# Performance work log

Hardware: AMD Instinct MI355X
Metric: run time of the kernel (lower is better)

Reference implementation:

```python
import jax, jax.numpy as jnp
import numpy as np

B, N, IN_NF, EDGE_NF = 2, 512, 3, 1
DIM, HEADS, DHEAD, DEPTH = 256, 8, 32, 2
INNER = HEADS * DHEAD
SCALE = DHEAD ** -0.5


def _layernorm(x, g, b):
    m = jnp.mean(x, axis=-1, keepdims=True)
    v = jnp.mean((x - m) ** 2, axis=-1, keepdims=True)
    return (x - m) / jnp.sqrt(v + 1e-5) * g + b


def _rotate_half(x):
    x1, x2 = jnp.split(x, 2, axis=-1)
    return jnp.concatenate([-x2, x1], axis=-1)


def _rotary_freqs(n):
    inv_freq = 1.0 / (10000.0 ** (jnp.arange(0, DHEAD, 2, dtype=jnp.float32) / DHEAD))
    f = jnp.einsum('i,j->ij', jnp.arange(n, dtype=jnp.float32), inv_freq)
    return jnp.concatenate([f, f], axis=-1)  # [n, DHEAD]


def _apply_rotary(freqs, t):
    return t * jnp.cos(freqs) + _rotate_half(t) * jnp.sin(freqs)


def _cdist(x):
    # pairwise L2 distances with grad-safe sqrt at zero (matches torch.cdist fwd)
    d2 = jnp.sum((x[:, :, None, :] - x[:, None, :, :]) ** 2, axis=-1)
    safe = jnp.where(d2 > 0.0, d2, 1.0)
    return jnp.where(d2 > 0.0, jnp.sqrt(safe), 0.0)


def setup_inputs():
    key = jax.random.key(0)
    ks = jax.random.split(key, 12)
    w = lambda k, *shape: jax.random.normal(k, shape, dtype=jnp.float32) * 0.02
    return dict(
        x=jax.random.normal(ks[0], (B, N, IN_NF), dtype=jnp.float32),
        t=jax.random.uniform(ks[1], (B, N, 1), dtype=jnp.float32),
        W_enc=w(ks[2], IN_NF + 1, DIM),
        W_dec=w(ks[3], DIM, IN_NF),
        ln_g=jnp.ones((DEPTH, DIM), jnp.float32),
        ln_b=jnp.zeros((DEPTH, DIM), jnp.float32),
        Wq=w(ks[4], DEPTH, DIM, INNER),
        bq=jnp.zeros((DEPTH, INNER), jnp.float32),
        Wkv=w(ks[5], DEPTH, DIM, 2 * INNER),
        bkv=jnp.zeros((DEPTH, 2 * INNER), jnp.float32),
        We=w(ks[6], DEPTH, EDGE_NF, INNER),
        be=jnp.zeros((DEPTH, INNER), jnp.float32),
        Wo=w(ks[7], DEPTH, INNER, DIM),
        bo=jnp.zeros((DEPTH, DIM), jnp.float32),
        Wg=w(ks[8], DEPTH, 3 * DIM, 1),
    )


def _forward(x, t, W_enc, W_dec, ln_g, ln_b, Wq, bq, Wkv, bkv, We, be, Wo, bo, Wg):
    b, n, _ = x.shape
    edges = _cdist(x)[..., None]                         # [B,N,N,1]
    nodes = jnp.concatenate([x, t], axis=-1) @ W_enc     # [B,N,DIM]
    freqs = _rotary_freqs(n)
    for l in range(DEPTH):
        h = _layernorm(nodes, ln_g[l], ln_b[l])          # PreNorm
        q = (h @ Wq[l] + bq[l]).reshape(b, n, HEADS, DHEAD).transpose(0, 2, 1, 3)
        k, v = jnp.split(h @ Wkv[l] + bkv[l], 2, axis=-1)
        k = k.reshape(b, n, HEADS, DHEAD).transpose(0, 2, 1, 3)
        v = v.reshape(b, n, HEADS, DHEAD).transpose(0, 2, 1, 3)
        e = (edges @ We[l] + be[l]).reshape(b, n, n, HEADS, DHEAD)  # [B,i,j,H,D]
        q = _apply_rotary(freqs, q)
        k = _apply_rotary(freqs, k)
        # sim = q . (k_j + e_ij); split to avoid an extra [B,H,N,N,D] materialization
        sim = (jnp.einsum('bhid,bhjd->bhij', q, k)
               + jnp.einsum('bhid,bijhd->bhij', q, e)) * SCALE
        attn = jax.nn.softmax(sim, axis=-1)
        # out = attn . (v_j + e_ij)
        out = (jnp.einsum('bhij,bhjd->bhid', attn, v)
               + jnp.einsum('bhij,bijhd->bhid', attn, e))
        out = out.transpose(0, 2, 1, 3).reshape(b, n, INNER) @ Wo[l] + bo[l]
        # gated residual
        gate = jax.nn.sigmoid(
            jnp.concatenate([out, nodes, out - nodes], axis=-1) @ Wg[l])
        nodes = out * gate + nodes * (1.0 - gate)
    return nodes @ W_dec                                  # [B,N,IN_NF]


def reference(x, t, W_enc, W_dec, ln_g, ln_b, Wq, bq, Wkv, bkv, We, be, Wo, bo, Wg):
    return _forward(x, t, W_enc, W_dec, ln_g, ln_b, Wq, bq, Wkv, bkv, We, be, Wo, bo, Wg)
```

## Files before the change

kernel.cpp:

```cpp
#include <hip/hip_runtime.h>
#include <math.h>

#define B 2
#define N 512
#define DIM 256
#define HEADS 8
#define DHEAD 32
#define INNER 256
#define DEPTH 2
#define SCALE 0.17677669529663687f

__device__ __forceinline__ float block_sum256(float v, float* red4) {
    #pragma unroll
    for (int o = 32; o; o >>= 1) v += __shfl_xor(v, o);
    int tid = threadIdx.x;
    __syncthreads();
    if ((tid & 63) == 0) red4[tid >> 6] = v;
    __syncthreads();
    return red4[0] + red4[1] + red4[2] + red4[3];
}

__global__ void k_tables(float* __restrict__ ct, float* __restrict__ st) {
    int idx = blockIdx.x * 256 + threadIdx.x;
    int i = idx >> 4, jj = idx & 15;
    double invf = pow(10000.0, -(double)jj / 16.0);
    double ang = (double)i * invf;
    ct[idx] = (float)cos(ang);
    st[idx] = (float)sin(ang);
}

__global__ void k_encode_ln(const float* __restrict__ x, const float* __restrict__ t,
                            const float* __restrict__ Wenc,
                            const float* __restrict__ ln_g, const float* __restrict__ ln_b,
                            float* __restrict__ nodes, float* __restrict__ hbuf) {
    __shared__ float red4[4];
    int row = blockIdx.x, d = threadIdx.x;
    float x0 = x[row*3+0], x1 = x[row*3+1], x2 = x[row*3+2], tt = t[row];
    float nv = x0*Wenc[d] + x1*Wenc[DIM+d] + x2*Wenc[2*DIM+d] + tt*Wenc[3*DIM+d];
    nodes[row*DIM + d] = nv;
    float mean = block_sum256(nv, red4) * (1.0f/DIM);
    float c = nv - mean;
    float var = block_sum256(c*c, red4) * (1.0f/DIM);
    hbuf[row*DIM + d] = c * (1.0f/sqrtf(var + 1e-5f)) * ln_g[d] + ln_b[d];
}

__global__ void k_dist(const float* __restrict__ x, float* __restrict__ dist) {
    int b = blockIdx.x / N, i = blockIdx.x % N, j = threadIdx.x;
    const float* xi = x + (b*N+i)*3;
    const float* xj = x + (b*N+j)*3;
    float d0 = xi[0]-xj[0], d1 = xi[1]-xj[1], d2 = xi[2]-xj[2];
    float s = d0*d0 + d1*d1 + d2*d2;
    dist[(size_t)(b*N+i)*N + j] = (s > 0.f) ? sqrtf(s) : 0.f;
}

__global__ __launch_bounds__(256, 4)
void k_gemm_qkv(const float* __restrict__ hbuf,
                const float* __restrict__ Wq, const float* __restrict__ bq,
                const float* __restrict__ Wkv, const float* __restrict__ bkv,
                const float* __restrict__ We, const float* __restrict__ be,
                const float* __restrict__ ct, const float* __restrict__ st,
                float* __restrict__ qbuf, float* __restrict__ kbuf, float* __restrict__ vbuf,
                float* __restrict__ qwe, float* __restrict__ qbe, int layer) {
    __shared__ float AT[64][32];
    __shared__ float Bs[64][64];

    int tid = threadIdx.x;
    int mt = blockIdx.x & 31;
    int nt = blockIdx.x >> 5;
    int tx = tid & 15, ty = tid >> 4;
    int n0 = nt * 64;

    const float* Wsrc; int wstride;
    if (n0 < 256) { Wsrc = Wq  + (size_t)layer*256*256 + n0;        wstride = 256; }
    else          { Wsrc = Wkv + (size_t)layer*256*512 + (n0-256);  wstride = 512; }

    float acc[2][4] = {{0,0,0,0},{0,0,0,0}};

    int am = tid & 31, ak = tid >> 5;
    int bn4 = tid & 15, bk = tid >> 4;

    for (int kt = 0; kt < 4; ++kt) {
        int kbase = kt * 64;
        if (kt) __syncthreads();
        {
            const float* src = hbuf + (size_t)(mt*32 + am)*256 + kbase + ak*8;
            float4 a0 = *(const float4*)src;
            float4 a1 = *(const float4*)(src + 4);
            AT[ak*8+0][am]=a0.x; AT[ak*8+1][am]=a0.y; AT[ak*8+2][am]=a0.z; AT[ak*8+3][am]=a0.w;
            AT[ak*8+4][am]=a1.x; AT[ak*8+5][am]=a1.y; AT[ak*8+6][am]=a1.z; AT[ak*8+7][am]=a1.w;
        }
        #pragma unroll
        for (int p = 0; p < 4; ++p) {
            int k = bk + p*16;
            float4 v = *(const float4*)(Wsrc + (size_t)(kbase + k)*wstride + bn4*4);
            *(float4*)&Bs[k][bn4*4] = v;
        }
        __syncthreads();
        #pragma unroll 8
        for (int k = 0; k < 64; ++k) {
            float2 a = *(const float2*)&AT[k][ty*2];
            float4 b = *(const float4*)&Bs[k][tx*4];
            acc[0][0] += a.x*b.x; acc[0][1] += a.x*b.y; acc[0][2] += a.x*b.z; acc[0][3] += a.x*b.w;
            acc[1][0] += a.y*b.x; acc[1][1] += a.y*b.y; acc[1][2] += a.y*b.z; acc[1][3] += a.y*b.w;
        }
    }

    int row = mt*32 + ty*2;
    int n = n0 + tx*4;

    float4 bias4;
    if (n0 < 256) bias4 = *(const float4*)&bq[layer*256 + n];
    else          bias4 = *(const float4*)&bkv[layer*512 + (n - 256)];
    #pragma unroll
    for (int r = 0; r < 2; ++r) {
        acc[r][0] += bias4.x; acc[r][1] += bias4.y; acc[r][2] += bias4.z; acc[r][3] += bias4.w;
    }

    if (n0 >= 512) {
        #pragma unroll
        for (int r = 0; r < 2; ++r) {
            float4 o = make_float4(acc[r][0], acc[r][1], acc[r][2], acc[r][3]);
            *(float4*)&vbuf[(size_t)(row + r)*256 + (n - 512)] = o;
        }
        return;
    }

    float* sh = &Bs[0][0];
    __syncthreads();
    #pragma unroll
    for (int r = 0; r < 2; ++r)
        #pragma unroll
        for (int c = 0; c < 4; ++c)
            sh[(ty*2 + r)*68 + tx*4 + c] = acc[r][c];
    __syncthreads();

    float wep[2] = {0.f, 0.f}, bep[2] = {0.f, 0.f};
    float val[2][4];
    #pragma unroll
    for (int r = 0; r < 2; ++r) {
        int ii = (row + r) & (N-1);
        #pragma unroll
        for (int c = 0; c < 4; ++c) {
            int tc = tx*4 + c;
            int dd = tc & 31, jj = tc & 15;
            float ca = ct[ii*16 + jj], sa = st[ii*16 + jj];
            int ptc = (dd < 16) ? tc + 16 : tc - 16;
            float sgn = (dd < 16) ? -1.f : 1.f;
            float partner = sh[(ty*2 + r)*68 + ptc];
            float rot = acc[r][c]*ca + sgn*partner*sa;
            val[r][c] = rot;
            if (n0 < 256) {
                wep[r] += rot * We[layer*256 + n0 + tc];
                bep[r] += rot * be[layer*256 + n0 + tc];
            }
        }
    }

    float* dst = (n0 < 256) ? qbuf : kbuf;
    int coln = (n0 < 256) ? n : n - 256;
    #pragma unroll
    for (int r = 0; r < 2; ++r) {
        float4 o = make_float4(val[r][0], val[r][1], val[r][2], val[r][3]);
        *(float4*)&dst[(size_t)(row + r)*256 + coln] = o;
    }

    if (n0 < 256) {
        #pragma unroll
        for (int r = 0; r < 2; ++r) {
            wep[r] += __shfl_xor(wep[r], 1); bep[r] += __shfl_xor(bep[r], 1);
            wep[r] += __shfl_xor(wep[r], 2); bep[r] += __shfl_xor(bep[r], 2);
            wep[r] += __shfl_xor(wep[r], 4); bep[r] += __shfl_xor(bep[r], 4);
        }
        if ((tid & 7) == 0) {
            int h = nt*2 + (tx >> 3);
            int bb = row >> 9;
            #pragma unroll
            for (int r = 0; r < 2; ++r) {
                int ii = (row + r) & (N-1);
                qwe[(bb*HEADS + h)*N + ii] = wep[r];
                qbe[(bb*HEADS + h)*N + ii] = bep[r];
            }
        }
    }
}

#define TI 8
__global__ __launch_bounds__(256, 4)
void k_attn(const float* __restrict__ qbuf, const float* __restrict__ kbuf,
            const float* __restrict__ vbuf,
            const float* __restrict__ qwe, const float* __restrict__ qbe,
            const float* __restrict__ dist,
            const float* __restrict__ We, const float* __restrict__ be,
            float* __restrict__ attnout, int layer) {
    __shared__ float Tt[32 * 128];

    int t = threadIdx.x;
    int g = t & 31;
    int r = t >> 5;
    int bid = blockIdx.x;
    int itile = bid & 63;
    int h = (bid >> 6) & (HEADS-1);
    int b = bid >> 9;
    int i = itile * TI + r;

    int scol = t & 127;
    int d0   = (t >> 7) * 16;

    float q[32];
    {
        const float4* qp = (const float4*)(qbuf + (size_t)(b*N + i) * INNER + h * DHEAD);
        #pragma unroll
        for (int c = 0; c < 8; ++c) {
            float4 v = qp[c];
            q[c*4+0] = v.x; q[c*4+1] = v.y; q[c*4+2] = v.z; q[c*4+3] = v.w;
        }
    }
    float qw = qwe[(b*HEADS + h)*N + i];
    float qb = qbe[(b*HEADS + h)*N + i];

    const float* kbase = kbuf + (size_t)b*N*INNER + h*DHEAD;
    const float* vbase = vbuf + (size_t)b*N*INNER + h*DHEAD;
    const float* drow  = dist + (size_t)(b*N + i) * N;

    float sim[16];

    #pragma unroll
    for (int jt = 0; jt < 4; ++jt) {
        if (jt) __syncthreads();
        {
            const float* src = kbase + (size_t)(jt*128 + scol) * INNER + d0;
            float4 a0 = *(const float4*)(src + 0);
            float4 a1 = *(const float4*)(src + 4);
            float4 a2 = *(const float4*)(src + 8);
            float4 a3 = *(const float4*)(src + 12);
            Tt[(d0+ 0)*128 + scol] = a0.x; Tt[(d0+ 1)*128 + scol] = a0.y;
            Tt[(d0+ 2)*128 + scol] = a0.z; Tt[(d0+ 3)*128 + scol] = a0.w;
            Tt[(d0+ 4)*128 + scol] = a1.x; Tt[(d0+ 5)*128 + scol] = a1.y;
            Tt[(d0+ 6)*128 + scol] = a1.z; Tt[(d0+ 7)*128 + scol] = a1.w;
            Tt[(d0+ 8)*128 + scol] = a2.x; Tt[(d0+ 9)*128 + scol] = a2.y;
            Tt[(d0+10)*128 + scol] = a2.z; Tt[(d0+11)*128 + scol] = a2.w;
            Tt[(d0+12)*128 + scol] = a3.x; Tt[(d0+13)*128 + scol] = a3.y;
            Tt[(d0+14)*128 + scol] = a3.z; Tt[(d0+15)*128 + scol] = a3.w;
        }
        __syncthreads();
        float4 s4 = make_float4(0.f,0.f,0.f,0.f);
        #pragma unroll
        for (int d = 0; d < 32; ++d) {
            float4 kv = *(const float4*)&Tt[d*128 + g*4];
            float qd = q[d];
            s4.x += qd*kv.x; s4.y += qd*kv.y; s4.z += qd*kv.z; s4.w += qd*kv.w;
        }
        float4 dv = *(const float4*)&drow[jt*128 + g*4];
        sim[jt*4+0] = (s4.x + dv.x*qw + qb) * SCALE;
        sim[jt*4+1] = (s4.y + dv.y*qw + qb) * SCALE;
        sim[jt*4+2] = (s4.z + dv.z*qw + qb) * SCALE;
        sim[jt*4+3] = (s4.w + dv.w*qw + qb) * SCALE;
    }

    float mx = -1e30f;
    #pragma unroll
    for (int v = 0; v < 16; ++v) mx = fmaxf(mx, sim[v]);
    mx = fmaxf(mx, __shfl_xor(mx, 1));
    mx = fmaxf(mx, __shfl_xor(mx, 2));
    mx = fmaxf(mx, __shfl_xor(mx, 4));
    mx = fmaxf(mx, __shfl_xor(mx, 8));
    mx = fmaxf(mx, __shfl_xor(mx, 16));

    float lsum = 0.f, ldsum = 0.f;
    #pragma unroll
    for (int jt = 0; jt < 4; ++jt) {
        float4 dv = *(const float4*)&drow[jt*128 + g*4];
        float dvv[4] = {dv.x, dv.y, dv.z, dv.w};
        #pragma unroll
        for (int u = 0; u < 4; ++u) {
            float p = __expf(sim[jt*4+u] - mx);
            sim[jt*4+u] = p;
            lsum  += p;
            ldsum += p * dvv[u];
        }
    }
    lsum += __shfl_xor(lsum, 1);  ldsum += __shfl_xor(ldsum, 1);
    lsum += __shfl_xor(lsum, 2);  ldsum += __shfl_xor(ldsum, 2);
    lsum += __shfl_xor(lsum, 4);  ldsum += __shfl_xor(ldsum, 4);
    lsum += __shfl_xor(lsum, 8);  ldsum += __shfl_xor(ldsum, 8);
    lsum += __shfl_xor(lsum, 16); ldsum += __shfl_xor(ldsum, 16);

    float acc[32];
    #pragma unroll
    for (int d = 0; d < 32; ++d) acc[d] = 0.f;

    #pragma unroll
    for (int jt = 0; jt < 4; ++jt) {
        __syncthreads();
        {
            const float* src = vbase + (size_t)(jt*128 + scol) * INNER + d0;
            float4 a0 = *(const float4*)(src + 0);
            float4 a1 = *(const float4*)(src + 4);
            float4 a2 = *(const float4*)(src + 8);
            float4 a3 = *(const float4*)(src + 12);
            Tt[(d0+ 0)*128 + scol] = a0.x; Tt[(d0+ 1)*128 + scol] = a0.y;
            Tt[(d0+ 2)*128 + scol] = a0.z; Tt[(d0+ 3)*128 + scol] = a0.w;
            Tt[(d0+ 4)*128 + scol] = a1.x; Tt[(d0+ 5)*128 + scol] = a1.y;
            Tt[(d0+ 6)*128 + scol] = a1.z; Tt[(d0+ 7)*128 + scol] = a1.w;
            Tt[(d0+ 8)*128 + scol] = a2.x; Tt[(d0+ 9)*128 + scol] = a2.y;
            Tt[(d0+10)*128 + scol] = a2.z; Tt[(d0+11)*128 + scol] = a2.w;
            Tt[(d0+12)*128 + scol] = a3.x; Tt[(d0+13)*128 + scol] = a3.y;
            Tt[(d0+14)*128 + scol] = a3.z; Tt[(d0+15)*128 + scol] = a3.w;
        }
        __syncthreads();
        float p0 = sim[jt*4+0], p1 = sim[jt*4+1], p2 = sim[jt*4+2], p3 = sim[jt*4+3];
        #pragma unroll
        for (int d = 0; d < 32; ++d) {
            float4 vv = *(const float4*)&Tt[d*128 + g*4];
            acc[d] += p0*vv.x + p1*vv.y + p2*vv.z + p3*vv.w;
        }
    }

    #pragma unroll
    for (int d = 0; d < 32; ++d) {
        acc[d] += __shfl_xor(acc[d], 1);
        acc[d] += __shfl_xor(acc[d], 2);
        acc[d] += __shfl_xor(acc[d], 4);
        acc[d] += __shfl_xor(acc[d], 8);
        acc[d] += __shfl_xor(acc[d], 16);
    }

    float invl = 1.0f / lsum;
    float ad = ldsum * invl;
    float o = acc[0];
    #pragma unroll
    for (int d = 1; d < 32; ++d) if (g == d) o = acc[d];
    o = o * invl + ad * We[layer*INNER + h*DHEAD + g] + be[layer*INNER + h*DHEAD + g];
    attnout[(size_t)(b*N + i)*INNER + h*DHEAD + g] = o;
}

__global__ __launch_bounds__(256, 4)
void k_gemm_o(const float* __restrict__ attnout, const float* __restrict__ Wo,
              const float* __restrict__ bo, float* __restrict__ obuf, int layer) {
    __shared__ float AT[64][32];
    __shared__ float Bs[64][32];
    int tid = threadIdx.x;
    int mt = blockIdx.x & 31, nt = blockIdx.x >> 5;
    int tx = tid & 7, ty = tid >> 3;

    float acc[4] = {0,0,0,0};
    int am = tid & 31, ak = tid >> 5;
    int bn4 = tid & 7, bk = tid >> 3;
    const float* Wsrc = Wo + (size_t)layer*256*256 + nt*32;

    for (int kt = 0; kt < 4; ++kt) {
        int kbase = kt * 64;
        if (kt) __syncthreads();
        {
            const float* src = attnout + (size_t)(mt*32 + am)*256 + kbase + ak*8;
            float4 a0 = *(const float4*)src;
            float4 a1 = *(const float4*)(src + 4);
            AT[ak*8+0][am]=a0.x; AT[ak*8+1][am]=a0.y; AT[ak*8+2][am]=a0.z; AT[ak*8+3][am]=a0.w;
            AT[ak*8+4][am]=a1.x; AT[ak*8+5][am]=a1.y; AT[ak*8+6][am]=a1.z; AT[ak*8+7][am]=a1.w;
        }
        #pragma unroll
        for (int p = 0; p < 2; ++p) {
            int k = bk + p*32;
            *(float4*)&Bs[k][bn4*4] = *(const float4*)(Wsrc + (size_t)(kbase + k)*256 + bn4*4);
        }
        __syncthreads();
        #pragma unroll 8
        for (int k = 0; k < 64; ++k) {
            float a = AT[k][ty];
            float4 b = *(const float4*)&Bs[k][tx*4];
            acc[0] += a*b.x; acc[1] += a*b.y; acc[2] += a*b.z; acc[3] += a*b.w;
        }
    }
    int row = mt*32 + ty, n = nt*32 + tx*4;
    float4 bias = *(const float4*)&bo[layer*256 + n];
    float4 o = make_float4(acc[0]+bias.x, acc[1]+bias.y, acc[2]+bias.z, acc[3]+bias.w);
    *(float4*)&obuf[(size_t)row*256 + n] = o;
}

__global__ void k_gate_ln(const float* __restrict__ obuf, const float* __restrict__ Wg,
                          const float* __restrict__ ln_g, const float* __restrict__ ln_b,
                          const float* __restrict__ Wdec,
                          float* __restrict__ nodes, float* __restrict__ hbuf,
                          float* __restrict__ out, int layer) {
    __shared__ float red4[4];
    int row = blockIdx.x, d = threadIdx.x;
    float o  = obuf[row*DIM + d];
    float nd = nodes[row*DIM + d];
    const float* Wgl = Wg + layer*3*DIM;
    float s = o*Wgl[d] + nd*Wgl[DIM+d] + (o-nd)*Wgl[2*DIM+d];
    float tot = block_sum256(s, red4);
    float gate = 1.0f/(1.0f + __expf(-tot));
    float nn = o*gate + nd*(1.0f - gate);
    nodes[row*DIM + d] = nn;
    if (layer == 0) {
        float mean = block_sum256(nn, red4) * (1.0f/DIM);
        float c = nn - mean;
        float var = block_sum256(c*c, red4) * (1.0f/DIM);
        hbuf[row*DIM + d] = c * (1.0f/sqrtf(var + 1e-5f)) * ln_g[DIM + d] + ln_b[DIM + d];
    } else {
        float s0 = block_sum256(nn * Wdec[d*3+0], red4);
        float s1 = block_sum256(nn * Wdec[d*3+1], red4);
        float s2 = block_sum256(nn * Wdec[d*3+2], red4);
        if (d == 0) { out[row*3+0] = s0; out[row*3+1] = s1; out[row*3+2] = s2; }
    }
}

extern "C" void kernel_launch(void* const* d_in, const int* in_sizes, int n_in,
                              void* d_out, int out_size, void* d_ws, size_t ws_size,
                              hipStream_t stream) {
    const float* x     = (const float*)d_in[0];
    const float* t     = (const float*)d_in[1];
    const float* W_enc = (const float*)d_in[2];
    const float* W_dec = (const float*)d_in[3];
    const float* ln_g  = (const float*)d_in[4];
    const float* ln_b  = (const float*)d_in[5];
    const float* Wq    = (const float*)d_in[6];
    const float* bq    = (const float*)d_in[7];
    const float* Wkv   = (const float*)d_in[8];
    const float* bkv   = (const float*)d_in[9];
    const float* We    = (const float*)d_in[10];
    const float* be    = (const float*)d_in[11];
    const float* Wo    = (const float*)d_in[12];
    const float* bo    = (const float*)d_in[13];
    const float* Wg    = (const float*)d_in[14];
    float* out = (float*)d_out;

    float* ws = (float*)d_ws;
    float* nodes   = ws;
    float* dist    = nodes   + B*N*DIM;
    float* hbuf    = dist    + B*N*N;
    float* qbuf    = hbuf    + B*N*DIM;
    float* kbuf    = qbuf    + B*N*INNER;
    float* vbuf    = kbuf    + B*N*INNER;
    float* qwe     = vbuf    + B*N*INNER;
    float* qbe     = qwe     + B*HEADS*N;
    float* attnout = qbe     + B*HEADS*N;
    float* obuf    = attnout + B*N*INNER;
    float* ct      = obuf    + B*N*DIM;
    float* st      = ct      + N*16;

    k_tables   <<<32,   256, 0, stream>>>(ct, st);
    k_encode_ln<<<B*N,  DIM, 0, stream>>>(x, t, W_enc, ln_g, ln_b, nodes, hbuf);
    k_dist     <<<B*N,  N,   0, stream>>>(x, dist);
    for (int l = 0; l < DEPTH; ++l) {
        k_gemm_qkv<<<384, 256, 0, stream>>>(hbuf, Wq, bq, Wkv, bkv, We, be, ct, st,
                                            qbuf, kbuf, vbuf, qwe, qbe, l);
        k_attn<<<B*HEADS*(N/TI), 256, 0, stream>>>(qbuf, kbuf, vbuf, qwe, qbe, dist, We, be,
                                                   attnout, l);
        k_gemm_o<<<256, 256, 0, stream>>>(attnout, Wo, bo, obuf, l);
        k_gate_ln<<<B*N, DIM, 0, stream>>>(obuf, Wg, ln_g, ln_b, W_dec, nodes, hbuf, out, l);
    }
}
```

Measured before the change: 129.6 us.

## Merge preprocessing kernels and process two query rows per attention thread

Three setup kernels (rotary tables, encode+layernorm, pairwise distance) are merged into one launch, with x staged in shared memory for the distance computation. The attention kernel now handles 16 query rows per block, each thread owning two rows, so every K/V tile staged in shared memory is reused twice and the block count is halved. The goal is fewer launches and less K/V reload traffic. In exchange, register pressure roughly doubles (launch bounds lowered to 2 blocks per CU) and fewer blocks are available to fill the GPU.

New measurement: 112.9 us. 1.15x faster.

```diff
diff --git a/kernel.cpp b/kernel.cpp
--- a/kernel.cpp
+++ b/kernel.cpp
@@ -20,21 +20,26 @@
     return red4[0] + red4[1] + red4[2] + red4[3];
 }
 
-__global__ void k_tables(float* __restrict__ ct, float* __restrict__ st) {
-    int idx = blockIdx.x * 256 + threadIdx.x;
-    int i = idx >> 4, jj = idx & 15;
-    double invf = pow(10000.0, -(double)jj / 16.0);
-    double ang = (double)i * invf;
-    ct[idx] = (float)cos(ang);
-    st[idx] = (float)sin(ang);
-}
-
-__global__ void k_encode_ln(const float* __restrict__ x, const float* __restrict__ t,
-                            const float* __restrict__ Wenc,
-                            const float* __restrict__ ln_g, const float* __restrict__ ln_b,
-                            float* __restrict__ nodes, float* __restrict__ hbuf) {
+__global__ void k_pre(const float* __restrict__ x, const float* __restrict__ t,
+                      const float* __restrict__ Wenc,
+                      const float* __restrict__ ln_g, const float* __restrict__ ln_b,
+                      float* __restrict__ nodes, float* __restrict__ hbuf,
+                      float* __restrict__ dist,
+                      float* __restrict__ ct, float* __restrict__ st) {
     __shared__ float red4[4];
+    __shared__ float xs[N * 3];
     int row = blockIdx.x, d = threadIdx.x;
+    int b = row >> 9, i = row & (N - 1);
+
+    if (blockIdx.x < 32) {
+        int idx = blockIdx.x * 256 + d;
+        int ii = idx >> 4, jj = idx & 15;
+        double invf = pow(10000.0, -(double)jj / 16.0);
+        double ang = (double)ii * invf;
+        ct[idx] = (float)cos(ang);
+        st[idx] = (float)sin(ang);
+    }
+
     float x0 = x[row*3+0], x1 = x[row*3+1], x2 = x[row*3+2], tt = t[row];
     float nv = x0*Wenc[d] + x1*Wenc[DIM+d] + x2*Wenc[2*DIM+d] + tt*Wenc[3*DIM+d];
     nodes[row*DIM + d] = nv;
@@ -42,15 +47,15 @@
     float c = nv - mean;
     float var = block_sum256(c*c, red4) * (1.0f/DIM);
     hbuf[row*DIM + d] = c * (1.0f/sqrtf(var + 1e-5f)) * ln_g[d] + ln_b[d];
-}
-
-__global__ void k_dist(const float* __restrict__ x, float* __restrict__ dist) {
-    int b = blockIdx.x / N, i = blockIdx.x % N, j = threadIdx.x;
-    const float* xi = x + (b*N+i)*3;
-    const float* xj = x + (b*N+j)*3;
-    float d0 = xi[0]-xj[0], d1 = xi[1]-xj[1], d2 = xi[2]-xj[2];
-    float s = d0*d0 + d1*d1 + d2*d2;
-    dist[(size_t)(b*N+i)*N + j] = (s > 0.f) ? sqrtf(s) : 0.f;
+
+    for (int f = d; f < N*3; f += 256) xs[f] = x[b*N*3 + f];
+    __syncthreads();
+    float xi0 = xs[i*3+0], xi1 = xs[i*3+1], xi2 = xs[i*3+2];
+    for (int j = d; j < N; j += 256) {
+        float d0 = xi0 - xs[j*3+0], d1 = xi1 - xs[j*3+1], d2 = xi2 - xs[j*3+2];
+        float s = d0*d0 + d1*d1 + d2*d2;
+        dist[(size_t)row*N + j] = (s > 0.f) ? sqrtf(s) : 0.f;
+    }
 }
 
 __global__ __launch_bounds__(256, 4)
@@ -184,8 +189,8 @@
     }
 }
 
-#define TI 8
-__global__ __launch_bounds__(256, 4)
+#define TI 16
+__global__ __launch_bounds__(256, 2)
 void k_attn(const float* __restrict__ qbuf, const float* __restrict__ kbuf,
             const float* __restrict__ vbuf,
             const float* __restrict__ qwe, const float* __restrict__ qbe,
@@ -198,31 +203,35 @@
     int g = t & 31;
     int r = t >> 5;
     int bid = blockIdx.x;
-    int itile = bid & 63;
-    int h = (bid >> 6) & (HEADS-1);
-    int b = bid >> 9;
-    int i = itile * TI + r;
+    int itile = bid & 31;
+    int h = (bid >> 5) & (HEADS-1);
+    int b = bid >> 8;
+    int i0 = itile * TI + r;
+    int i1 = i0 + 8;
 
     int scol = t & 127;
     int d0   = (t >> 7) * 16;
 
-    float q[32];
+    float q0[32], q1[32];
     {
-        const float4* qp = (const float4*)(qbuf + (size_t)(b*N + i) * INNER + h * DHEAD);
+        const float4* qp0 = (const float4*)(qbuf + (size_t)(b*N + i0) * INNER + h * DHEAD);
+        const float4* qp1 = (const float4*)(qbuf + (size_t)(b*N + i1) * INNER + h * DHEAD);
         #pragma unroll
         for (int c = 0; c < 8; ++c) {
-            float4 v = qp[c];
-            q[c*4+0] = v.x; q[c*4+1] = v.y; q[c*4+2] = v.z; q[c*4+3] = v.w;
-        }
-    }
-    float qw = qwe[(b*HEADS + h)*N + i];
-    float qb = qbe[(b*HEADS + h)*N + i];
+            float4 v0 = qp0[c], v1 = qp1[c];
+            q0[c*4+0] = v0.x; q0[c*4+1] = v0.y; q0[c*4+2] = v0.z; q0[c*4+3] = v0.w;
+            q1[c*4+0] = v1.x; q1[c*4+1] = v1.y; q1[c*4+2] = v1.z; q1[c*4+3] = v1.w;
+        }
+    }
+    float qw0 = qwe[(b*HEADS + h)*N + i0], qb0 = qbe[(b*HEADS + h)*N + i0];
+    float qw1 = qwe[(b*HEADS + h)*N + i1], qb1 = qbe[(b*HEADS + h)*N + i1];
 
     const float* kbase = kbuf + (size_t)b*N*INNER + h*DHEAD;
     const float* vbase = vbuf + (size_t)b*N*INNER + h*DHEAD;
-    const float* drow  = dist + (size_t)(b*N + i) * N;
-
-    float sim[16];
+    const float* drow0 = dist + (size_t)(b*N + i0) * N;
+    const float* drow1 = dist + (size_t)(b*N + i1) * N;
+
+    float sim0[16], sim1[16];
 
     #pragma unroll
     for (int jt = 0; jt < 4; ++jt) {
@@ -243,51 +252,61 @@
             Tt[(d0+14)*128 + scol] = a3.z; Tt[(d0+15)*128 + scol] = a3.w;
         }
         __syncthreads();
-        float4 s4 = make_float4(0.f,0.f,0.f,0.f);
+        float4 s0 = make_float4(0.f,0.f,0.f,0.f);
+        float4 s1 = make_float4(0.f,0.f,0.f,0.f);
         #pragma unroll
         for (int d = 0; d < 32; ++d) {
             float4 kv = *(const float4*)&Tt[d*128 + g*4];
-            float qd = q[d];
-            s4.x += qd*kv.x; s4.y += qd*kv.y; s4.z += qd*kv.z; s4.w += qd*kv.w;
-        }
-        float4 dv = *(const float4*)&drow[jt*128 + g*4];
-        sim[jt*4+0] = (s4.x + dv.x*qw + qb) * SCALE;
-        sim[jt*4+1] = (s4.y + dv.y*qw + qb) * SCALE;
-        sim[jt*4+2] = (s4.z + dv.z*qw + qb) * SCALE;
-        sim[jt*4+3] = (s4.w + dv.w*qw + qb) * SCALE;
-    }
-
-    float mx = -1e30f;
-    #pragma unroll
-    for (int v = 0; v < 16; ++v) mx = fmaxf(mx, sim[v]);
-    mx = fmaxf(mx, __shfl_xor(mx, 1));
-    mx = fmaxf(mx, __shfl_xor(mx, 2));
-    mx = fmaxf(mx, __shfl_xor(mx, 4));
-    mx = fmaxf(mx, __shfl_xor(mx, 8));
-    mx = fmaxf(mx, __shfl_xor(mx, 16));
-
-    float lsum = 0.f, ldsum = 0.f;
+            float qa = q0[d], qc = q1[d];
+            s0.x += qa*kv.x; s0.y += qa*kv.y; s0.z += qa*kv.z; s0.w += qa*kv.w;
+            s1.x += qc*kv.x; s1.y += qc*kv.y; s1.z += qc*kv.z; s1.w += qc*kv.w;
+        }
+        float4 dv0 = *(const float4*)&drow0[jt*128 + g*4];
+        float4 dv1 = *(const float4*)&drow1[jt*128 + g*4];
+        sim0[jt*4+0] = (s0.x + dv0.x*qw0 + qb0) * SCALE;
+        sim0[jt*4+1] = (s0.y + dv0.y*qw0 + qb0) * SCALE;
+        sim0[jt*4+2] = (s0.z + dv0.z*qw0 + qb0) * SCALE;
+        sim0[jt*4+3] = (s0.w + dv0.w*qw0 + qb0) * SCALE;
+        sim1[jt*4+0] = (s1.x + dv1.x*qw1 + qb1) * SCALE;
+        sim1[jt*4+1] = (s1.y + dv1.y*qw1 + qb1) * SCALE;
+        sim1[jt*4+2] = (s1.z + dv1.z*qw1 + qb1) * SCALE;
+        sim1[jt*4+3] = (s1.w + dv1.w*qw1 + qb1) * SCALE;
+    }
+
+    float mx0 = -1e30f, mx1 = -1e30f;
+    #pragma unroll
+    for (int v = 0; v < 16; ++v) { mx0 = fmaxf(mx0, sim0[v]); mx1 = fmaxf(mx1, sim1[v]); }
+    #pragma unroll
+    for (int o = 1; o <= 16; o <<= 1) {
+        mx0 = fmaxf(mx0, __shfl_xor(mx0, o));
+        mx1 = fmaxf(mx1, __shfl_xor(mx1, o));
+    }
+
+    float ls0 = 0.f, ld0 = 0.f, ls1 = 0.f, ld1 = 0.f;
     #pragma unroll
     for (int jt = 0; jt < 4; ++jt) {
-        float4 dv = *(const float4*)&drow[jt*128 + g*4];
-        float dvv[4] = {dv.x, dv.y, dv.z, dv.w};
+        float4 dv0 = *(const float4*)&drow0[jt*128 + g*4];
+        float4 dv1 = *(const float4*)&drow1[jt*128 + g*4];
+        float a0[4] = {dv0.x,dv0.y,dv0.z,dv0.w};
+        float a1[4] = {dv1.x,dv1.y,dv1.z,dv1.w};
         #pragma unroll
         for (int u = 0; u < 4; ++u) {
-            float p = __expf(sim[jt*4+u] - mx);
-            sim[jt*4+u] = p;
-            lsum  += p;
-            ldsum += p * dvv[u];
-        }
-    }
-    lsum += __shfl_xor(lsum, 1);  ldsum += __shfl_xor(ldsum, 1);
-    lsum += __shfl_xor(lsum, 2);  ldsum += __shfl_xor(ldsum, 2);
-    lsum += __shfl_xor(lsum, 4);  ldsum += __shfl_xor(ldsum, 4);
-    lsum += __shfl_xor(lsum, 8);  ldsum += __shfl_xor(ldsum, 8);
-    lsum += __shfl_xor(lsum, 16); ldsum += __shfl_xor(ldsum, 16);
-
-    float acc[32];
-    #pragma unroll
-    for (int d = 0; d < 32; ++d) acc[d] = 0.f;
+            float p0 = __expf(sim0[jt*4+u] - mx0);
+            float p1 = __expf(sim1[jt*4+u] - mx1);
+            sim0[jt*4+u] = p0; sim1[jt*4+u] = p1;
+            ls0 += p0; ld0 += p0 * a0[u];
+            ls1 += p1; ld1 += p1 * a1[u];
+        }
+    }
+    #pragma unroll
+    for (int o = 1; o <= 16; o <<= 1) {
+        ls0 += __shfl_xor(ls0, o); ld0 += __shfl_xor(ld0, o);
+        ls1 += __shfl_xor(ls1, o); ld1 += __shfl_xor(ld1, o);
+    }
+
+    float acc0[32], acc1[32];
+    #pragma unroll
+    for (int d = 0; d < 32; ++d) { acc0[d] = 0.f; acc1[d] = 0.f; }
 
     #pragma unroll
     for (int jt = 0; jt < 4; ++jt) {
@@ -308,30 +327,34 @@
             Tt[(d0+14)*128 + scol] = a3.z; Tt[(d0+15)*128 + scol] = a3.w;
         }
         __syncthreads();
-        float p0 = sim[jt*4+0], p1 = sim[jt*4+1], p2 = sim[jt*4+2], p3 = sim[jt*4+3];
+        float p00 = sim0[jt*4+0], p01 = sim0[jt*4+1], p02 = sim0[jt*4+2], p03 = sim0[jt*4+3];
+        float p10 = sim1[jt*4+0], p11 = sim1[jt*4+1], p12 = sim1[jt*4+2], p13 = sim1[jt*4+3];
         #pragma unroll
         for (int d = 0; d < 32; ++d) {
             float4 vv = *(const float4*)&Tt[d*128 + g*4];
-            acc[d] += p0*vv.x + p1*vv.y + p2*vv.z + p3*vv.w;
+            acc0[d] += p00*vv.x + p01*vv.y + p02*vv.z + p03*vv.w;
+            acc1[d] += p10*vv.x + p11*vv.y + p12*vv.z + p13*vv.w;
         }
     }
 
     #pragma unroll
     for (int d = 0; d < 32; ++d) {
-        acc[d] += __shfl_xor(acc[d], 1);
-        acc[d] += __shfl_xor(acc[d], 2);
-        acc[d] += __shfl_xor(acc[d], 4);
-        acc[d] += __shfl_xor(acc[d], 8);
-        acc[d] += __shfl_xor(acc[d], 16);
-    }
-
-    float invl = 1.0f / lsum;
-    float ad = ldsum * invl;
-    float o = acc[0];
-    #pragma unroll
-    for (int d = 1; d < 32; ++d) if (g == d) o = acc[d];
-    o = o * invl + ad * We[layer*INNER + h*DHEAD + g] + be[layer*INNER + h*DHEAD + g];
-    attnout[(size_t)(b*N + i)*INNER + h*DHEAD + g] = o;
+        #pragma unroll
+        for (int o = 1; o <= 16; o <<= 1) {
+            acc0[d] += __shfl_xor(acc0[d], o);
+            acc1[d] += __shfl_xor(acc1[d], o);
+        }
+    }
+
+    float il0 = 1.0f / ls0, il1 = 1.0f / ls1;
+    float ad0 = ld0 * il0, ad1 = ld1 * il1;
+    float o0 = acc0[0], o1 = acc1[0];
+    #pragma unroll
+    for (int d = 1; d < 32; ++d) if (g == d) { o0 = acc0[d]; o1 = acc1[d]; }
+    float wv = We[layer*INNER + h*DHEAD + g];
+    float bv = be[layer*INNER + h*DHEAD + g];
+    attnout[(size_t)(b*N + i0)*INNER + h*DHEAD + g] = o0*il0 + ad0*wv + bv;
+    attnout[(size_t)(b*N + i1)*INNER + h*DHEAD + g] = o1*il1 + ad1*wv + bv;
 }
 
 __global__ __launch_bounds__(256, 4)
@@ -439,9 +462,7 @@
     float* ct      = obuf    + B*N*DIM;
     float* st      = ct      + N*16;
 
-    k_tables   <<<32,   256, 0, stream>>>(ct, st);
-    k_encode_ln<<<B*N,  DIM, 0, stream>>>(x, t, W_enc, ln_g, ln_b, nodes, hbuf);
-    k_dist     <<<B*N,  N,   0, stream>>>(x, dist);
+    k_pre<<<B*N, DIM, 0, stream>>>(x, t, W_enc, ln_g, ln_b, nodes, hbuf, dist, ct, st);
     for (int l = 0; l < DEPTH; ++l) {
         k_gemm_qkv<<<384, 256, 0, stream>>>(hbuf, Wq, bq, Wkv, bkv, We, be, ct, st,
                                             qbuf, kbuf, vbuf, qwe, qbe, l);
```
